# Kernel optimization log

Hardware: AMD Instinct MI355X
Metric: run time of the kernel (lower is better)

Reference implementation:

```python
import jax, jax.numpy as jnp
import numpy as np

NV, NE = 4096, 8192
FV, FE = 128, 64
FV_OUT = 128


def setup_inputs() -> dict:
    key = jax.random.key(0)
    ks = jax.random.split(key, 8)
    stdv = 1.0 / np.sqrt(FV_OUT)
    return {
        "H_v": jax.random.normal(ks[0], (NV, FV), dtype=jnp.float32),
        "H_e": jax.random.normal(ks[1], (NE, FE), dtype=jnp.float32),
        "adj_e": jax.random.uniform(ks[2], (NE, NE), dtype=jnp.float32),
        "adj_v": jax.random.uniform(ks[3], (NV, NV), dtype=jnp.float32),
        "T": jax.random.uniform(ks[4], (NV, NE), dtype=jnp.float32),
        "weight": jax.random.uniform(ks[5], (FV, FV_OUT), minval=-stdv, maxval=stdv, dtype=jnp.float32),
        "p": jax.random.normal(ks[6], (1, FE), dtype=jnp.float32),
        "bias": jax.random.uniform(ks[7], (FV_OUT,), minval=-stdv, maxval=stdv, dtype=jnp.float32),
    }


def reference(H_v, H_e, adj_e, adj_v, T, weight, p, bias):
    # node_layer=True path of GraphConvolution.forward
    # d = (H_e @ p.T) as a vector over edges; T @ diag(d) == T * d[None, :]
    d = (H_e @ p.T)[:, 0]                       # [Ne]
    multiplier = (T * d[None, :]) @ T.T         # [Nv, Nv]
    n = multiplier.shape[0]
    mask = jnp.eye(n, dtype=multiplier.dtype)   # eye mask: diag -> 1, off-diag -> multiplier
    M1 = mask + (1.0 - mask) * multiplier
    adjusted_A = M1 * adj_v                     # elementwise mask with dense adjacency
    output = adjusted_A @ (H_v @ weight) + bias # [Nv, Fv_out]
    return (output, H_e)
```

## Files before the change

### kernel.cpp

```cpp
#include <hip/hip_runtime.h>
#include <stdint.h>

#define NV 4096
#define NE 8192
#define FV 128
#define FE 64
#define FOUT 128

typedef unsigned short u16;
typedef __attribute__((ext_vector_type(8))) short short8;
typedef __attribute__((ext_vector_type(4))) float f32x4;
typedef __attribute__((ext_vector_type(4))) unsigned short u16x4;

__device__ __forceinline__ u16 f2bf(float f) {
  uint32_t u = __builtin_bit_cast(uint32_t, f);
  u += 0x7fffu + ((u >> 16) & 1u);
  return (u16)(u >> 16);
}
__device__ __forceinline__ float bf2f(u16 h) {
  return __builtin_bit_cast(float, (uint32_t)h << 16);
}

#define AS1(p) ((__attribute__((address_space(1))) void*)(void*)(p))
#define AS3(p) ((__attribute__((address_space(3))) void*)(p))

__global__ __launch_bounds__(64) void k_edge_dot(const float* __restrict__ He,
                                                 const float* __restrict__ p,
                                                 float* __restrict__ d) {
  int e = blockIdx.x;
  int l = threadIdx.x;
  float v = He[e * FE + l] * p[l];
  #pragma unroll
  for (int off = 32; off > 0; off >>= 1) v += __shfl_down(v, off);
  if (l == 0) d[e] = v;
}

__global__ __launch_bounds__(256) void k_convert(const float* __restrict__ T,
                                                 const float* __restrict__ d,
                                                 u16* __restrict__ Ta,
                                                 u16* __restrict__ Tb) {
  size_t idx = ((size_t)blockIdx.x * 256 + threadIdx.x) * 4;
  f32x4 t = *(const f32x4*)&T[idx];
  int e = (int)(idx & (NE - 1));
  f32x4 dv = *(const f32x4*)&d[e];
  u16x4 a, b;
  a.x = f2bf(t.x * dv.x); a.y = f2bf(t.y * dv.y);
  a.z = f2bf(t.z * dv.z); a.w = f2bf(t.w * dv.w);
  b.x = f2bf(t.x); b.y = f2bf(t.y); b.z = f2bf(t.z); b.w = f2bf(t.w);
  *(u16x4*)&Ta[idx] = a;
  *(u16x4*)&Tb[idx] = b;
}

__global__ __launch_bounds__(128) void k_hw(const float* __restrict__ Hv,
                                            const float* __restrict__ W,
                                            u16* __restrict__ HWt) {
  __shared__ float sh[FV];
  int i = blockIdx.x;
  int n = threadIdx.x;
  sh[n] = Hv[i * FV + n];
  __syncthreads();
  float s = 0.f;
  #pragma unroll
  for (int f = 0; f < FV; ++f) s += sh[f] * W[f * FOUT + n];
  HWt[(size_t)n * NV + i] = f2bf(s);
}

__global__ __launch_bounds__(256) void k_init_out(float* __restrict__ out,
                                                  const float* __restrict__ bias,
                                                  const float* __restrict__ He) {
  int idx = blockIdx.x * 256 + threadIdx.x;
  if (idx < NV * FOUT) out[idx] = bias[idx & (FOUT - 1)];
  else out[idx] = He[idx - NV * FOUT];
}

__global__ __launch_bounds__(512, 2) void k_gemm_m(const u16* __restrict__ Ta,
                                                   const u16* __restrict__ Tb,
                                                   const float* __restrict__ adjv,
                                                   u16* __restrict__ adjA) {
  __shared__ __align__(16) u16 smem[65536];

  const int bi = blockIdx.x >> 4;
  const int bj = blockIdx.x & 15;
  const int tile_m = bi * 256;
  const int tile_n = bj * 256;
  const int tid = threadIdx.x;
  const int lane = tid & 63;
  const int wid = tid >> 6;
  const int wr = wid >> 2;
  const int wc = wid & 3;
  const int row16 = lane & 15;
  const int quad = lane >> 4;
  const int swz8 = (quad ^ ((row16 >> 1) & 3)) * 8;

  const int srow = tid >> 2;
  const int sslot = (tid & 3) ^ ((tid >> 3) & 3);
  const u16* gA0 = Ta + (size_t)(tile_m + srow) * NE + sslot * 8;
  const u16* gA1 = gA0 + (size_t)128 * NE;
  const u16* gB0 = Tb + (size_t)(tile_n + srow) * NE + sslot * 8;
  const u16* gB1 = gB0 + (size_t)128 * NE;
  const int ldsO0 = (wid * 64) * 8;
  const int ldsO1 = (512 + wid * 64) * 8;

#define STG(gp0, gp1, roff, kcol)                                                                 \
  do {                                                                                            \
    __builtin_amdgcn_global_load_lds(AS1((gp0) + (kcol)), AS3(&smem[(roff) + ldsO0]), 16, 0, 0);  \
    __builtin_amdgcn_global_load_lds(AS1((gp1) + (kcol)), AS3(&smem[(roff) + ldsO1]), 16, 0, 0);  \
  } while (0)

  f32x4 acc[8][4] = {};
  short8 aF[8], bF[2];

  const int arow32 = (wr * 128 + row16) * 32 + swz8;
  const int brow32 = (wc * 64 + row16) * 32 + swz8;

#define LDA(b, kk)                                                                \
  do { _Pragma("unroll")                                                          \
    for (int mi = 0; mi < 8; ++mi)                                                \
      aF[mi] = *(const short8*)&smem[(b)*16384 + (kk)*8192 + arow32 + mi * 512];  \
  } while (0)

#define LDB(b, kk, nh)                                                                             \
  do { _Pragma("unroll")                                                                           \
    for (int nn = 0; nn < 2; ++nn)                                                                 \
      bF[nn] = *(const short8*)&smem[32768 + (b)*16384 + (kk)*8192 + brow32 + ((nh)*2+nn) * 512];  \
  } while (0)

#define MM(nh)                                                                                              \
  do { _Pragma("unroll")                                                                                    \
    for (int mi = 0; mi < 8; ++mi) {                                                                        \
      acc[mi][(nh)*2+0] = __builtin_amdgcn_mfma_f32_16x16x32_bf16(aF[mi], bF[0], acc[mi][(nh)*2+0], 0,0,0); \
      acc[mi][(nh)*2+1] = __builtin_amdgcn_mfma_f32_16x16x32_bf16(aF[mi], bF[1], acc[mi][(nh)*2+1], 0,0,0); \
    }                                                                                                       \
  } while (0)

#define BAR()   __builtin_amdgcn_s_barrier()
#define LGKM0() do { asm volatile("s_waitcnt lgkmcnt(0)" ::: "memory"); \
                     __builtin_amdgcn_sched_barrier(0); } while (0)
#define VM6()   asm volatile("s_waitcnt vmcnt(6)" ::: "memory")
#define PRIO1() __builtin_amdgcn_s_setprio(1)
#define PRIO0() __builtin_amdgcn_s_setprio(0)

  STG(gA0, gA1, 0,             0);
  STG(gB0, gB1, 32768,         0);
  STG(gA0, gA1, 8192,          32);
  STG(gB0, gB1, 32768 + 8192,  32);
  STG(gA0, gA1, 16384,         64);
  STG(gB0, gB1, 32768 + 16384, 64);
  STG(gA0, gA1, 16384 + 8192,  96);
  VM6();
  BAR();

  for (int it = 0; it < 64; ++it) {
    const int t = it * 2;
    const int k1 = (t + 1) * 64;
    const int k2 = (t + 2 < 128 ? t + 2 : 127) * 64;
    const int k3 = (t + 3 < 128 ? t + 3 : 127) * 64;

    LDA(0, 0); LDB(0, 0, 0);
    STG(gB0, gB1, 32768 + 16384 + 8192, k1 + 32);
    BAR(); LGKM0();
    PRIO1(); MM(0); PRIO0();
    BAR();

    LDB(0, 0, 1);
    STG(gA0, gA1, 0, k2);
    BAR(); LGKM0();
    PRIO1(); MM(1); PRIO0();
    BAR();

    LDA(0, 1); LDB(0, 1, 0);
    STG(gB0, gB1, 32768, k2);
    BAR(); LGKM0();
    PRIO1(); MM(0); PRIO0();
    BAR();

    LDB(0, 1, 1);
    STG(gA0, gA1, 8192, k2 + 32);
    BAR(); LGKM0();
    PRIO1(); MM(1); PRIO0();
    VM6();
    BAR();

    LDA(1, 0); LDB(1, 0, 0);
    STG(gB0, gB1, 32768 + 8192, k2 + 32);
    BAR(); LGKM0();
    PRIO1(); MM(0); PRIO0();
    BAR();

    LDB(1, 0, 1);
    STG(gA0, gA1, 16384, k3);
    BAR(); LGKM0();
    PRIO1(); MM(1); PRIO0();
    BAR();

    LDA(1, 1); LDB(1, 1, 0);
    STG(gB0, gB1, 32768 + 16384, k3);
    BAR(); LGKM0();
    PRIO1(); MM(0); PRIO0();
    BAR();

    LDB(1, 1, 1);
    STG(gA0, gA1, 16384 + 8192, k3 + 32);
    BAR(); LGKM0();
    PRIO1(); MM(1); PRIO0();
    VM6();
    BAR();
  }

  #pragma unroll
  for (int mi = 0; mi < 8; ++mi) {
    const int gr0 = tile_m + wr * 128 + mi * 16 + quad * 4;
    #pragma unroll
    for (int ni = 0; ni < 4; ++ni) {
      const int gc = tile_n + wc * 64 + ni * 16 + row16;
      #pragma unroll
      for (int r = 0; r < 4; ++r) {
        const int gr = gr0 + r;
        float v = acc[mi][ni][r];
        v = (gr == gc) ? 1.0f : v;
        v *= adjv[(size_t)gr * NV + gc];
        adjA[(size_t)gr * NV + gc] = f2bf(v);
      }
    }
  }

#undef STG
#undef LDA
#undef LDB
#undef MM
#undef BAR
#undef LGKM0
#undef VM6
#undef PRIO1
#undef PRIO0
}

#define KSPLIT 16
__global__ __launch_bounds__(256) void k_gemm_out(const u16* __restrict__ A,
                                                  const u16* __restrict__ B,
                                                  float* __restrict__ out) {
  __shared__ __align__(16) u16 lA[128 * 32];
  __shared__ __align__(16) u16 lB[128 * 32];
  const int K = NV;
  const int tile_m = blockIdx.y * 128;
  const int kbeg = blockIdx.x * (K / KSPLIT);
  const int kend = kbeg + (K / KSPLIT);
  const int tid = threadIdx.x;
  const int lane = tid & 63;
  const int wave = tid >> 6;
  const int wm = (wave >> 1) * 64;
  const int wn = (wave & 1) * 64;
  const int row16 = lane & 15;
  const int quad = lane >> 4;

  f32x4 acc[4][4] = {};

  for (int k0 = kbeg; k0 < kend; k0 += 32) {
    __syncthreads();
    #pragma unroll
    for (int r = 0; r < 2; ++r) {
      const int chunk = r * 256 + wave * 64 + lane;
      const int row = chunk >> 2;
      const int cc = chunk & 3;
      const u16* ga = A + ((size_t)(tile_m + row) * K + k0 + cc * 8);
      const u16* gb = B + ((size_t)row * K + k0 + cc * 8);
      __builtin_amdgcn_global_load_lds(AS1(ga), AS3(&lA[(r * 256 + wave * 64) * 8]), 16, 0, 0);
      __builtin_amdgcn_global_load_lds(AS1(gb), AS3(&lB[(r * 256 + wave * 64) * 8]), 16, 0, 0);
    }
    __syncthreads();
    short8 a[4], b[4];
    #pragma unroll
    for (int mi = 0; mi < 4; ++mi)
      a[mi] = *(const short8*)&lA[(wm + mi * 16 + row16) * 32 + quad * 8];
    #pragma unroll
    for (int ni = 0; ni < 4; ++ni)
      b[ni] = *(const short8*)&lB[(wn + ni * 16 + row16) * 32 + quad * 8];
    #pragma unroll
    for (int mi = 0; mi < 4; ++mi)
      #pragma unroll
      for (int ni = 0; ni < 4; ++ni)
        acc[mi][ni] = __builtin_amdgcn_mfma_f32_16x16x32_bf16(a[mi], b[ni], acc[mi][ni], 0, 0, 0);
  }

  #pragma unroll
  for (int mi = 0; mi < 4; ++mi) {
    #pragma unroll
    for (int ni = 0; ni < 4; ++ni) {
      const int gc = wn + ni * 16 + row16;
      #pragma unroll
      for (int r = 0; r < 4; ++r) {
        const int gr = tile_m + wm + mi * 16 + quad * 4 + r;
        atomicAdd(&out[(size_t)gr * FOUT + gc], acc[mi][ni][r]);
      }
    }
  }
}

extern "C" void kernel_launch(void* const* d_in, const int* in_sizes, int n_in,
                              void* d_out, int out_size, void* d_ws, size_t ws_size,
                              hipStream_t stream) {
  const float* Hv   = (const float*)d_in[0];
  const float* He   = (const float*)d_in[1];
  const float* adjv = (const float*)d_in[3];
  const float* T    = (const float*)d_in[4];
  const float* W    = (const float*)d_in[5];
  const float* p    = (const float*)d_in[6];
  const float* bias = (const float*)d_in[7];
  float* out = (float*)d_out;

  char* ws = (char*)d_ws;
  float* dvec = (float*)ws;
  u16* HWt  = (u16*)(ws + ((size_t)1 << 20));
  u16* Ta   = (u16*)(ws + ((size_t)2 << 20));
  u16* Tb   = (u16*)(ws + ((size_t)2 << 20) + ((size_t)64 << 20));
  u16* adjA = (u16*)(ws + ((size_t)2 << 20) + ((size_t)128 << 20));

  k_edge_dot<<<NE, 64, 0, stream>>>(He, p, dvec);
  k_convert<<<(NV * NE) / (256 * 4), 256, 0, stream>>>(T, dvec, Ta, Tb);
  k_hw<<<NV, 128, 0, stream>>>(Hv, W, HWt);
  k_init_out<<<(NV * FOUT + NE * FE) / 256, 256, 0, stream>>>(out, bias, He);
  k_gemm_m<<<256, 512, 0, stream>>>(Ta, Tb, adjv, adjA);
  k_gemm_out<<<dim3(KSPLIT, NV / 128), 256, 0, stream>>>(adjA, HWt, out);
}
```

Before: 720.0 us.

## Coalesce GEMM epilogue via LDS, replace atomics with split-K reduce, widen helper kernels

The multiplier GEMM now stages its accumulator tile through shared memory, so the adjacency mask and bf16 store run as coalesced vector accesses. Its inner loop is reordered to load four A and four B fragments per step instead of eight and two. The output GEMM writes per-split partials that a separate reduce kernel sums with the bias, replacing atomics. Helper kernels (edge dot, convert, H_v@W, H_e copy) are widened or vectorised. In exchange there is extra workspace traffic for partials, one more launch, and a larger LDS footprint.

```diff
diff --git a/kernel.cpp b/kernel.cpp
--- a/kernel.cpp
+++ b/kernel.cpp
@@ -24,60 +24,81 @@
 #define AS1(p) ((__attribute__((address_space(1))) void*)(void*)(p))
 #define AS3(p) ((__attribute__((address_space(3))) void*)(p))
 
-__global__ __launch_bounds__(64) void k_edge_dot(const float* __restrict__ He,
-                                                 const float* __restrict__ p,
-                                                 float* __restrict__ d) {
-  int e = blockIdx.x;
-  int l = threadIdx.x;
-  float v = He[e * FE + l] * p[l];
-  #pragma unroll
-  for (int off = 32; off > 0; off >>= 1) v += __shfl_down(v, off);
-  if (l == 0) d[e] = v;
+__global__ __launch_bounds__(256) void k_edge_dot(const float* __restrict__ He,
+                                                  const float* __restrict__ p,
+                                                  float* __restrict__ d) {
+  const int lane = threadIdx.x & 63;
+  const int gw = blockIdx.x * 4 + (threadIdx.x >> 6);
+  const float pv = p[lane];
+  for (int e = gw; e < NE; e += 512) {
+    float v = He[(size_t)e * FE + lane] * pv;
+    #pragma unroll
+    for (int off = 32; off > 0; off >>= 1) v += __shfl_down(v, off);
+    if (lane == 0) d[e] = v;
+  }
 }
 
 __global__ __launch_bounds__(256) void k_convert(const float* __restrict__ T,
                                                  const float* __restrict__ d,
                                                  u16* __restrict__ Ta,
                                                  u16* __restrict__ Tb) {
-  size_t idx = ((size_t)blockIdx.x * 256 + threadIdx.x) * 4;
-  f32x4 t = *(const f32x4*)&T[idx];
+  size_t idx = ((size_t)blockIdx.x * 256 + threadIdx.x) * 8;
+  f32x4 t0 = *(const f32x4*)&T[idx];
+  f32x4 t1 = *(const f32x4*)&T[idx + 4];
   int e = (int)(idx & (NE - 1));
-  f32x4 dv = *(const f32x4*)&d[e];
-  u16x4 a, b;
-  a.x = f2bf(t.x * dv.x); a.y = f2bf(t.y * dv.y);
-  a.z = f2bf(t.z * dv.z); a.w = f2bf(t.w * dv.w);
-  b.x = f2bf(t.x); b.y = f2bf(t.y); b.z = f2bf(t.z); b.w = f2bf(t.w);
-  *(u16x4*)&Ta[idx] = a;
-  *(u16x4*)&Tb[idx] = b;
-}
-
-__global__ __launch_bounds__(128) void k_hw(const float* __restrict__ Hv,
+  f32x4 d0 = *(const f32x4*)&d[e];
+  f32x4 d1 = *(const f32x4*)&d[e + 4];
+  short8 a, b;
+  a[0] = (short)f2bf(t0.x * d0.x); a[1] = (short)f2bf(t0.y * d0.y);
+  a[2] = (short)f2bf(t0.z * d0.z); a[3] = (short)f2bf(t0.w * d0.w);
+  a[4] = (short)f2bf(t1.x * d1.x); a[5] = (short)f2bf(t1.y * d1.y);
+  a[6] = (short)f2bf(t1.z * d1.z); a[7] = (short)f2bf(t1.w * d1.w);
+  b[0] = (short)f2bf(t0.x); b[1] = (short)f2bf(t0.y);
+  b[2] = (short)f2bf(t0.z); b[3] = (short)f2bf(t0.w);
+  b[4] = (short)f2bf(t1.x); b[5] = (short)f2bf(t1.y);
+  b[6] = (short)f2bf(t1.z); b[7] = (short)f2bf(t1.w);
+  *(short8*)&Ta[idx] = a;
+  *(short8*)&Tb[idx] = b;
+}
+
+__global__ __launch_bounds__(256) void k_hw(const float* __restrict__ Hv,
                                             const float* __restrict__ W,
                                             u16* __restrict__ HWt) {
-  __shared__ float sh[FV];
-  int i = blockIdx.x;
-  int n = threadIdx.x;
-  sh[n] = Hv[i * FV + n];
+  __shared__ float sW[FV * FOUT];
+  __shared__ float sH[8 * FV];
+  const int tid = threadIdx.x;
+  const int i0 = blockIdx.x * 8;
+  #pragma unroll
+  for (int k = 0; k < 16; ++k)
+    *(f32x4*)&sW[k * 1024 + tid * 4] = *(const f32x4*)&W[k * 1024 + tid * 4];
+  *(f32x4*)&sH[tid * 4] = *(const f32x4*)&Hv[(size_t)i0 * FV + tid * 4];
   __syncthreads();
-  float s = 0.f;
-  #pragma unroll
-  for (int f = 0; f < FV; ++f) s += sh[f] * W[f * FOUT + n];
-  HWt[(size_t)n * NV + i] = f2bf(s);
-}
-
-__global__ __launch_bounds__(256) void k_init_out(float* __restrict__ out,
-                                                  const float* __restrict__ bias,
-                                                  const float* __restrict__ He) {
-  int idx = blockIdx.x * 256 + threadIdx.x;
-  if (idx < NV * FOUT) out[idx] = bias[idx & (FOUT - 1)];
-  else out[idx] = He[idx - NV * FOUT];
+  const int n = tid & 127;
+  const int rh = tid >> 7;
+  float acc[4] = {0.f, 0.f, 0.f, 0.f};
+  #pragma unroll 4
+  for (int f = 0; f < FV; ++f) {
+    float wv = sW[f * FOUT + n];
+    #pragma unroll
+    for (int rr = 0; rr < 4; ++rr)
+      acc[rr] += sH[(rh * 4 + rr) * FV + f] * wv;
+  }
+  #pragma unroll
+  for (int rr = 0; rr < 4; ++rr)
+    HWt[(size_t)n * NV + i0 + rh * 4 + rr] = f2bf(acc[rr]);
+}
+
+__global__ __launch_bounds__(256) void k_copy_he(float* __restrict__ out,
+                                                 const float* __restrict__ He) {
+  size_t idx = ((size_t)blockIdx.x * 256 + threadIdx.x) * 4;
+  *(f32x4*)&out[(size_t)NV * FOUT + idx] = *(const f32x4*)&He[idx];
 }
 
 __global__ __launch_bounds__(512, 2) void k_gemm_m(const u16* __restrict__ Ta,
                                                    const u16* __restrict__ Tb,
                                                    const float* __restrict__ adjv,
                                                    u16* __restrict__ adjA) {
-  __shared__ __align__(16) u16 smem[65536];
+  __shared__ __align__(16) u16 smem[66560];
 
   const int bi = blockIdx.x >> 4;
   const int bj = blockIdx.x & 15;
@@ -108,28 +129,28 @@
   } while (0)
 
   f32x4 acc[8][4] = {};
-  short8 aF[8], bF[2];
+  short8 aF[4], bF[4];
 
   const int arow32 = (wr * 128 + row16) * 32 + swz8;
   const int brow32 = (wc * 64 + row16) * 32 + swz8;
 
-#define LDA(b, kk)                                                                \
-  do { _Pragma("unroll")                                                          \
-    for (int mi = 0; mi < 8; ++mi)                                                \
-      aF[mi] = *(const short8*)&smem[(b)*16384 + (kk)*8192 + arow32 + mi * 512];  \
+#define LDA4(b, kk, mh)                                                                        \
+  do { _Pragma("unroll")                                                                       \
+    for (int m2 = 0; m2 < 4; ++m2)                                                             \
+      aF[m2] = *(const short8*)&smem[(b)*16384 + (kk)*8192 + arow32 + ((mh)*4 + m2) * 512];    \
   } while (0)
 
-#define LDB(b, kk, nh)                                                                             \
-  do { _Pragma("unroll")                                                                           \
-    for (int nn = 0; nn < 2; ++nn)                                                                 \
-      bF[nn] = *(const short8*)&smem[32768 + (b)*16384 + (kk)*8192 + brow32 + ((nh)*2+nn) * 512];  \
+#define LDB4(b, kk)                                                                            \
+  do { _Pragma("unroll")                                                                       \
+    for (int ni = 0; ni < 4; ++ni)                                                             \
+      bF[ni] = *(const short8*)&smem[32768 + (b)*16384 + (kk)*8192 + brow32 + ni * 512];       \
   } while (0)
 
-#define MM(nh)                                                                                              \
+#define MMH(mh)                                                                                             \
   do { _Pragma("unroll")                                                                                    \
-    for (int mi = 0; mi < 8; ++mi) {                                                                        \
-      acc[mi][(nh)*2+0] = __builtin_amdgcn_mfma_f32_16x16x32_bf16(aF[mi], bF[0], acc[mi][(nh)*2+0], 0,0,0); \
-      acc[mi][(nh)*2+1] = __builtin_amdgcn_mfma_f32_16x16x32_bf16(aF[mi], bF[1], acc[mi][(nh)*2+1], 0,0,0); \
+    for (int m2 = 0; m2 < 4; ++m2) { _Pragma("unroll")                                                      \
+      for (int ni = 0; ni < 4; ++ni)                                                                        \
+        acc[(mh)*4+m2][ni] = __builtin_amdgcn_mfma_f32_16x16x32_bf16(aF[m2], bF[ni], acc[(mh)*4+m2][ni], 0,0,0); \
     }                                                                                                       \
   } while (0)
 
@@ -140,13 +161,13 @@
 #define PRIO1() __builtin_amdgcn_s_setprio(1)
 #define PRIO0() __builtin_amdgcn_s_setprio(0)
 
-  STG(gA0, gA1, 0,             0);
-  STG(gB0, gB1, 32768,         0);
-  STG(gA0, gA1, 8192,          32);
-  STG(gB0, gB1, 32768 + 8192,  32);
-  STG(gA0, gA1, 16384,         64);
-  STG(gB0, gB1, 32768 + 16384, 64);
-  STG(gA0, gA1, 16384 + 8192,  96);
+  STG(gA0, gA1, 0,     0);
+  STG(gB0, gB1, 32768, 0);
+  STG(gA0, gA1, 8192,  32);
+  STG(gB0, gB1, 40960, 32);
+  STG(gB0, gB1, 49152, 64);
+  STG(gA0, gA1, 16384, 64);
+  STG(gB0, gB1, 57344, 96);
   VM6();
   BAR();
 
@@ -156,78 +177,96 @@
     const int k2 = (t + 2 < 128 ? t + 2 : 127) * 64;
     const int k3 = (t + 3 < 128 ? t + 3 : 127) * 64;
 
-    LDA(0, 0); LDB(0, 0, 0);
-    STG(gB0, gB1, 32768 + 16384 + 8192, k1 + 32);
-    BAR(); LGKM0();
-    PRIO1(); MM(0); PRIO0();
-    BAR();
-
-    LDB(0, 0, 1);
+    LDB4(0, 0); LDA4(0, 0, 0);
+    STG(gA0, gA1, 24576, k1 + 32);
+    BAR(); LGKM0();
+    PRIO1(); MMH(0); PRIO0();
+    BAR();
+
+    LDA4(0, 0, 1);
+    STG(gB0, gB1, 32768, k2);
+    BAR(); LGKM0();
+    PRIO1(); MMH(1); PRIO0();
+    BAR();
+
+    LDB4(0, 1); LDA4(0, 1, 0);
     STG(gA0, gA1, 0, k2);
     BAR(); LGKM0();
-    PRIO1(); MM(1); PRIO0();
-    BAR();
-
-    LDA(0, 1); LDB(0, 1, 0);
-    STG(gB0, gB1, 32768, k2);
-    BAR(); LGKM0();
-    PRIO1(); MM(0); PRIO0();
-    BAR();
-
-    LDB(0, 1, 1);
+    PRIO1(); MMH(0); PRIO0();
+    BAR();
+
+    LDA4(0, 1, 1);
+    STG(gB0, gB1, 40960, k2 + 32);
+    BAR(); LGKM0();
+    PRIO1(); MMH(1); PRIO0();
+    VM6();
+    BAR();
+
+    LDB4(1, 0); LDA4(1, 0, 0);
     STG(gA0, gA1, 8192, k2 + 32);
     BAR(); LGKM0();
-    PRIO1(); MM(1); PRIO0();
+    PRIO1(); MMH(0); PRIO0();
+    BAR();
+
+    LDA4(1, 0, 1);
+    STG(gB0, gB1, 49152, k3);
+    BAR(); LGKM0();
+    PRIO1(); MMH(1); PRIO0();
+    BAR();
+
+    LDB4(1, 1); LDA4(1, 1, 0);
+    STG(gA0, gA1, 16384, k3);
+    BAR(); LGKM0();
+    PRIO1(); MMH(0); PRIO0();
+    BAR();
+
+    LDA4(1, 1, 1);
+    STG(gB0, gB1, 57344, k3 + 32);
+    BAR(); LGKM0();
+    PRIO1(); MMH(1); PRIO0();
     VM6();
     BAR();
-
-    LDA(1, 0); LDB(1, 0, 0);
-    STG(gB0, gB1, 32768 + 8192, k2 + 32);
-    BAR(); LGKM0();
-    PRIO1(); MM(0); PRIO0();
-    BAR();
-
-    LDB(1, 0, 1);
-    STG(gA0, gA1, 16384, k3);
-    BAR(); LGKM0();
-    PRIO1(); MM(1); PRIO0();
-    BAR();
-
-    LDA(1, 1); LDB(1, 1, 0);
-    STG(gB0, gB1, 32768 + 16384, k3);
-    BAR(); LGKM0();
-    PRIO1(); MM(0); PRIO0();
-    BAR();
-
-    LDB(1, 1, 1);
-    STG(gA0, gA1, 16384 + 8192, k3 + 32);
-    BAR(); LGKM0();
-    PRIO1(); MM(1); PRIO0();
-    VM6();
-    BAR();
-  }
-
+  }
+
+  asm volatile("s_waitcnt vmcnt(0)" ::: "memory");
+  __syncthreads();
   #pragma unroll
   for (int mi = 0; mi < 8; ++mi) {
-    const int gr0 = tile_m + wr * 128 + mi * 16 + quad * 4;
     #pragma unroll
     for (int ni = 0; ni < 4; ++ni) {
-      const int gc = tile_n + wc * 64 + ni * 16 + row16;
+      const int row = wr * 128 + mi * 16 + quad * 4;
+      const int col = wc * 64 + ni * 16 + row16;
       #pragma unroll
-      for (int r = 0; r < 4; ++r) {
-        const int gr = gr0 + r;
-        float v = acc[mi][ni][r];
-        v = (gr == gc) ? 1.0f : v;
-        v *= adjv[(size_t)gr * NV + gc];
-        adjA[(size_t)gr * NV + gc] = f2bf(v);
-      }
+      for (int r = 0; r < 4; ++r)
+        smem[(row + r) * 260 + col] = f2bf(acc[mi][ni][r]);
     }
   }
+  __syncthreads();
+  const int ep_r = tid >> 4;
+  const int ep_c = (tid & 15) * 4;
+  for (int pass = 0; pass < 8; ++pass) {
+    const int row = pass * 32 + ep_r;
+    const int gr = tile_m + row;
+    const size_t gbase = (size_t)gr * NV + tile_n;
+    #pragma unroll
+    for (int j = 0; j < 4; ++j) {
+      const int col = ep_c + j * 64;
+      const int gc = tile_n + col;
+      u16x4 m4 = *(const u16x4*)&smem[row * 260 + col];
+      f32x4 av = *(const f32x4*)&adjv[gbase + col];
+      u16x4 o;
+      o.x = f2bf(((gr == gc + 0) ? 1.0f : bf2f(m4.x)) * av.x);
+      o.y = f2bf(((gr == gc + 1) ? 1.0f : bf2f(m4.y)) * av.y);
+      o.z = f2bf(((gr == gc + 2) ? 1.0f : bf2f(m4.z)) * av.z);
+      o.w = f2bf(((gr == gc + 3) ? 1.0f : bf2f(m4.w)) * av.w);
+      *(u16x4*)&adjA[gbase + col] = o;
+    }
+  }
 
 #undef STG
-#undef LDA
-#undef LDB
-#undef MM
+#undef LDA4
+#undef LDB4
+#undef MMH
 #undef BAR
 #undef LGKM0
 #undef VM6
@@ -238,7 +277,7 @@
 #define KSPLIT 16
 __global__ __launch_bounds__(256) void k_gemm_out(const u16* __restrict__ A,
                                                   const u16* __restrict__ B,
-                                                  float* __restrict__ out) {
+                                                  float* __restrict__ part) {
   __shared__ __align__(16) u16 lA[128 * 32];
   __shared__ __align__(16) u16 lB[128 * 32];
   const int K = NV;
@@ -282,6 +321,7 @@
         acc[mi][ni] = __builtin_amdgcn_mfma_f32_16x16x32_bf16(a[mi], b[ni], acc[mi][ni], 0, 0, 0);
   }
 
+  float* pdst = part + (size_t)blockIdx.x * NV * FOUT;
   #pragma unroll
   for (int mi = 0; mi < 4; ++mi) {
     #pragma unroll
@@ -290,10 +330,21 @@
       #pragma unroll
       for (int r = 0; r < 4; ++r) {
         const int gr = tile_m + wm + mi * 16 + quad * 4 + r;
-        atomicAdd(&out[(size_t)gr * FOUT + gc], acc[mi][ni][r]);
+        pdst[(size_t)gr * FOUT + gc] = acc[mi][ni][r];
       }
     }
   }
+}
+
+__global__ __launch_bounds__(256) void k_reduce(const float* __restrict__ part,
+                                                const float* __restrict__ bias,
+                                                float* __restrict__ out) {
+  size_t idx = ((size_t)blockIdx.x * 256 + threadIdx.x) * 4;
+  f32x4 s = *(const f32x4*)&bias[idx & (FOUT - 1)];
+  #pragma unroll
+  for (int ks = 0; ks < KSPLIT; ++ks)
+    s += *(const f32x4*)&part[(size_t)ks * NV * FOUT + idx];
+  *(f32x4*)&out[idx] = s;
 }
 
 extern "C" void kernel_launch(void* const* d_in, const int* in_sizes, int n_in,
@@ -310,15 +361,17 @@
 
   char* ws = (char*)d_ws;
   float* dvec = (float*)ws;
-  u16* HWt  = (u16*)(ws + ((size_t)1 << 20));
-  u16* Ta   = (u16*)(ws + ((size_t)2 << 20));
-  u16* Tb   = (u16*)(ws + ((size_t)2 << 20) + ((size_t)64 << 20));
-  u16* adjA = (u16*)(ws + ((size_t)2 << 20) + ((size_t)128 << 20));
-
-  k_edge_dot<<<NE, 64, 0, stream>>>(He, p, dvec);
-  k_convert<<<(NV * NE) / (256 * 4), 256, 0, stream>>>(T, dvec, Ta, Tb);
-  k_hw<<<NV, 128, 0, stream>>>(Hv, W, HWt);
-  k_init_out<<<(NV * FOUT + NE * FE) / 256, 256, 0, stream>>>(out, bias, He);
+  u16* HWt    = (u16*)(ws + ((size_t)1 << 20));
+  u16* Ta     = (u16*)(ws + ((size_t)2 << 20));
+  u16* Tb     = (u16*)(ws + ((size_t)2 << 20) + ((size_t)64 << 20));
+  u16* adjA   = (u16*)(ws + ((size_t)2 << 20) + ((size_t)128 << 20));
+  float* part = (float*)(ws + ((size_t)2 << 20) + ((size_t)160 << 20));
+
+  k_edge_dot<<<128, 256, 0, stream>>>(He, p, dvec);
+  k_convert<<<(NV * NE) / (256 * 8), 256, 0, stream>>>(T, dvec, Ta, Tb);
+  k_hw<<<NV / 8, 256, 0, stream>>>(Hv, W, HWt);
+  k_copy_he<<<(NE * FE) / (256 * 4), 256, 0, stream>>>(out, He);
   k_gemm_m<<<256, 512, 0, stream>>>(Ta, Tb, adjv, adjA);
-  k_gemm_out<<<dim3(KSPLIT, NV / 128), 256, 0, stream>>>(adjA, HWt, out);
-}
+  k_gemm_out<<<dim3(KSPLIT, NV / 128), 256, 0, stream>>>(adjA, HWt, part);
+  k_reduce<<<(NV * FOUT) / (256 * 4), 256, 0, stream>>>(part, bias, out);
+}
```

New measurement: 688.9 us. -4.3%, faster.
